# Optimization experiments

Hardware: AMD Instinct MI355X
Metric: run time of the kernel (lower is better)

## Reference

```python
import jax, jax.numpy as jnp
import numpy as np

N, F_IN, F_OUT, K = 16384, 64, 64, 3


def setup_inputs() -> dict:
    key = jax.random.key(0)
    k1, k2, k3, k4 = jax.random.split(key, 4)
    x = jax.random.normal(k1, (N, F_IN), dtype=jnp.float32)
    # dense rescaled Laplacian; scale so repeated matmuls stay numerically tame
    L_tilde = jax.random.normal(k2, (N, N), dtype=jnp.float32) / np.float32(np.sqrt(N))
    stdv = 1.0 / np.sqrt(F_OUT)
    weights = jax.random.uniform(k3, (K + 1, F_IN, F_OUT), dtype=jnp.float32,
                                 minval=-stdv, maxval=stdv)
    bias = jax.random.uniform(k4, (F_OUT,), dtype=jnp.float32, minval=-stdv, maxval=stdv)
    return {"x": x, "L_tilde": L_tilde, "weights": weights, "bias": bias}


def reference(x, L_tilde, weights, bias):
    # Chebyshev recurrence: T0 = x, T1 = L@x, Tk = 2*L@T_{k-1} - T_{k-2}
    T_prev = x                                   # (N, F_in)
    out = T_prev @ weights[0]                    # (N, F_out)
    T_curr = L_tilde @ x
    out = out + T_curr @ weights[1]
    for k in range(2, K + 1):                    # fixed small K: python loop is fine
        T_next = 2.0 * (L_tilde @ T_curr) - T_prev
        out = out + T_next @ weights[k]
        T_prev, T_curr = T_curr, T_next
    return out + bias
```

## Files before the change

kernel.cpp:

```cpp
#include <hip/hip_runtime.h>
#include <cstddef>
#include <cstdint>

#define NN 16384
#define FF 64
#define BM 64
#define BK 64
#define SK 4
#define KQ (NN / SK)
#define NC (KQ / BK)

typedef __attribute__((ext_vector_type(8))) short bf16x8;
typedef __attribute__((ext_vector_type(4))) float f32x4;
typedef unsigned short ushort_t;

#define GLOBAL_AS __attribute__((address_space(1)))
#define LDS_AS    __attribute__((address_space(3)))

#define VMCNT8   asm volatile("s_waitcnt vmcnt(8)" ::: "memory")
#define VMCNT0   asm volatile("s_waitcnt vmcnt(0)" ::: "memory")
#define LGKMCNT0 asm volatile("s_waitcnt lgkmcnt(0)" ::: "memory")
#define SCHEDB   __builtin_amdgcn_sched_barrier(0)
#define BARRIER  __builtin_amdgcn_s_barrier()

__device__ __forceinline__ void f32_split(float f, ushort_t& h, ushort_t& l) {
    unsigned u = __builtin_bit_cast(unsigned, f);
    h = (ushort_t)(u >> 16);
    float hf = __builtin_bit_cast(float, u & 0xFFFF0000u);
    float lo = f - hf;
    l = (ushort_t)(__builtin_bit_cast(unsigned, lo) >> 16);
}

__global__ __launch_bounds__(256) void convT_init(
    const float* __restrict__ X, ushort_t* __restrict__ Th,
    ushort_t* __restrict__ Tl, const float* __restrict__ W0,
    const float* __restrict__ bias, float* __restrict__ out)
{
    __shared__ float S[64][68];
    __shared__ float W[64][64];
    const int t = threadIdx.x;
    const int rb = blockIdx.x * 64;
    {
        const int row = t >> 2;
        const int c0 = (t & 3) * 16;
        const float* src = X + (size_t)(rb + row) * FF + c0;
        *(float4*)&S[row][c0 + 0]  = *(const float4*)(src + 0);
        *(float4*)&S[row][c0 + 4]  = *(const float4*)(src + 4);
        *(float4*)&S[row][c0 + 8]  = *(const float4*)(src + 8);
        *(float4*)&S[row][c0 + 12] = *(const float4*)(src + 12);
        float4* wd = (float4*)&W[0][0];
        const float4* ws = (const float4*)W0;
#pragma unroll
        for (int j = 0; j < 4; ++j) wd[t * 4 + j] = ws[t * 4 + j];
    }
    __syncthreads();
    {
        const int cc = t >> 2;
        const int r0 = (t & 3) * 16;
        ushort_t hh[16], ll[16];
#pragma unroll
        for (int i = 0; i < 16; ++i) f32_split(S[r0 + i][cc], hh[i], ll[i]);
        unsigned wh[8], wl[8];
#pragma unroll
        for (int j = 0; j < 8; ++j) {
            wh[j] = (unsigned)hh[2 * j] | ((unsigned)hh[2 * j + 1] << 16);
            wl[j] = (unsigned)ll[2 * j] | ((unsigned)ll[2 * j + 1] << 16);
        }
        const size_t o = (size_t)cc * NN + rb + r0;
        *(uint4*)(Th + o)     = make_uint4(wh[0], wh[1], wh[2], wh[3]);
        *(uint4*)(Th + o + 8) = make_uint4(wh[4], wh[5], wh[6], wh[7]);
        *(uint4*)(Tl + o)     = make_uint4(wl[0], wl[1], wl[2], wl[3]);
        *(uint4*)(Tl + o + 8) = make_uint4(wl[4], wl[5], wl[6], wl[7]);
    }
    {
        const int row0 = (t >> 3) * 2;
        const int col0 = (t & 7) * 8;
        float acc[2][8];
        const float4 b0 = *(const float4*)(bias + col0);
        const float4 b1 = *(const float4*)(bias + col0 + 4);
#pragma unroll
        for (int r = 0; r < 2; ++r) {
            acc[r][0] = b0.x; acc[r][1] = b0.y; acc[r][2] = b0.z; acc[r][3] = b0.w;
            acc[r][4] = b1.x; acc[r][5] = b1.y; acc[r][6] = b1.z; acc[r][7] = b1.w;
        }
#pragma unroll
        for (int f = 0; f < FF; ++f) {
            const float x0 = S[row0][f];
            const float x1 = S[row0 + 1][f];
            const float4 w0 = *(const float4*)&W[f][col0];
            const float4 w1 = *(const float4*)&W[f][col0 + 4];
            acc[0][0] += x0 * w0.x; acc[0][1] += x0 * w0.y;
            acc[0][2] += x0 * w0.z; acc[0][3] += x0 * w0.w;
            acc[0][4] += x0 * w1.x; acc[0][5] += x0 * w1.y;
            acc[0][6] += x0 * w1.z; acc[0][7] += x0 * w1.w;
            acc[1][0] += x1 * w0.x; acc[1][1] += x1 * w0.y;
            acc[1][2] += x1 * w0.z; acc[1][3] += x1 * w0.w;
            acc[1][4] += x1 * w1.x; acc[1][5] += x1 * w1.y;
            acc[1][6] += x1 * w1.z; acc[1][7] += x1 * w1.w;
        }
#pragma unroll
        for (int r = 0; r < 2; ++r) {
            const size_t o = (size_t)(rb + row0 + r) * FF + col0;
            float4 v0, v1;
            v0.x = acc[r][0]; v0.y = acc[r][1]; v0.z = acc[r][2]; v0.w = acc[r][3];
            v1.x = acc[r][4]; v1.y = acc[r][5]; v1.z = acc[r][6]; v1.w = acc[r][7];
            *(float4*)(out + o) = v0;
            *(float4*)(out + o + 4) = v1;
        }
    }
}

__global__ __launch_bounds__(256) void cheb_gemm_mfma(
    const float* __restrict__ L, const ushort_t* __restrict__ Th,
    const ushort_t* __restrict__ Tl, float* __restrict__ P)
{
    __shared__ ushort_t Ah[2][BM * BK];
    __shared__ ushort_t Al[2][BM * BK];
    __shared__ ushort_t Bh[3][FF * BK];
    __shared__ ushort_t Bl[3][FF * BK];

    const int tid  = threadIdx.x;
    const int lane = tid & 63;
    const int w    = tid >> 6;
    const int s    = blockIdx.x >> 8;
    const int m    = blockIdx.x & 255;
    const int row0g = m * BM;
    const int kbase = s * KQ;

    const int wm = w >> 1, wn = w & 1;
    const int frow = lane & 15;
    const int fk8  = (lane >> 4) * 8;

    const int arow = w * 4 + (lane >> 4);
    const int akq  = lane & 15;
    const int axor = (arow & 7) << 4;

    const ushort_t* Tsrc = (w & 1) ? Tl : Th;
    const int boct0 = (w >> 1) * 4;

    f32x4 acc[2][2];
#pragma unroll
    for (int i = 0; i < 2; ++i)
#pragma unroll
        for (int j = 0; j < 2; ++j) acc[i][j] = (f32x4)0.f;

    float4 vaA[4], vaB[4];

    const float* Labase = L + (size_t)(row0g + arow) * NN + kbase + akq * 4;

#define ISSUE_B(c, sb)                                                          \
    {                                                                           \
        const size_t kc = (size_t)(c) * BK;                                     \
        char* bbase = (char*)((w & 1) ? Bl[sb] : Bh[sb]);                       \
        _Pragma("unroll")                                                       \
        for (int o = 0; o < 4; ++o) {                                           \
            const int oct = boct0 + o;                                          \
            const int col = oct * 8 + (lane >> 3);                              \
            const ushort_t* g = Tsrc + (size_t)col * NN + kbase + kc            \
                                + (((lane & 7) ^ (col & 7)) * 8);               \
            __builtin_amdgcn_global_load_lds((const GLOBAL_AS void*)g,          \
                (LDS_AS void*)(bbase + oct * 1024), 16, 0, 0);                  \
        }                                                                       \
    }

#define LOAD_A(va, c)                                                           \
    {                                                                           \
        const float* g = Labase + (size_t)(c) * BK;                             \
        va[0] = *(const float4*)(g);                                            \
        va[1] = *(const float4*)(g + (size_t)16 * NN);                          \
        va[2] = *(const float4*)(g + (size_t)32 * NN);                          \
        va[3] = *(const float4*)(g + (size_t)48 * NN);                          \
    }

#define CONV_WRITE_A(va, sa)                                                    \
    {                                                                           \
        char* ahb = (char*)Ah[sa];                                              \
        char* alb = (char*)Al[sa];                                              \
        _Pragma("unroll")                                                       \
        for (int p = 0; p < 4; ++p) {                                           \
            const int r = arow + p * 16;                                        \
            ushort_t h0, h1, h2, h3, l0, l1, l2, l3;                            \
            f32_split(va[p].x, h0, l0);                                         \
            f32_split(va[p].y, h1, l1);                                         \
            f32_split(va[p].z, h2, l2);                                         \
            f32_split(va[p].w, h3, l3);                                         \
            const unsigned hi01 = (unsigned)h0 | ((unsigned)h1 << 16);          \
            const unsigned hi23 = (unsigned)h2 | ((unsigned)h3 << 16);          \
            const unsigned lo01 = (unsigned)l0 | ((unsigned)l1 << 16);          \
            const unsigned lo23 = (unsigned)l2 | ((unsigned)l3 << 16);          \
            const int byte = (r * 128 + akq * 8) ^ axor;                        \
            *(uint2*)(ahb + byte) = make_uint2(hi01, hi23);                     \
            *(uint2*)(alb + byte) = make_uint2(lo01, lo23);                     \
        }                                                                       \
    }

#define COMPUTE(sa, sb)                                                         \
    {                                                                           \
        const char* ahb = (const char*)Ah[sa];                                  \
        const char* alb = (const char*)Al[sa];                                  \
        const char* bhb = (const char*)Bh[sb];                                  \
        const char* blb = (const char*)Bl[sb];                                  \
        _Pragma("unroll")                                                       \
        for (int ks = 0; ks < 2; ++ks) {                                        \
            const int kk = ks * 32 + fk8;                                       \
            bf16x8 Afh[2], Afl[2], Bfh[2], Bfl[2];                              \
            _Pragma("unroll")                                                   \
            for (int mt = 0; mt < 2; ++mt) {                                    \
                const int row = wm * 32 + mt * 16 + frow;                       \
                const int off = (row * 128 + kk * 2) ^ ((row & 7) << 4);        \
                Afh[mt] = *(const bf16x8*)(ahb + off);                          \
                Afl[mt] = *(const bf16x8*)(alb + off);                          \
            }                                                                   \
            _Pragma("unroll")                                                   \
            for (int nt = 0; nt < 2; ++nt) {                                    \
                const int col = wn * 32 + nt * 16 + frow;                       \
                const int off = (col * 128 + kk * 2) ^ ((col & 7) << 4);        \
                Bfh[nt] = *(const bf16x8*)(bhb + off);                          \
                Bfl[nt] = *(const bf16x8*)(blb + off);                          \
            }                                                                   \
            _Pragma("unroll")                                                   \
            for (int mt = 0; mt < 2; ++mt)                                      \
                _Pragma("unroll")                                               \
                for (int nt = 0; nt < 2; ++nt) {                                \
                    acc[mt][nt] = __builtin_amdgcn_mfma_f32_16x16x32_bf16(      \
                        Afh[mt], Bfh[nt], acc[mt][nt], 0, 0, 0);                \
                    acc[mt][nt] = __builtin_amdgcn_mfma_f32_16x16x32_bf16(      \
                        Afh[mt], Bfl[nt], acc[mt][nt], 0, 0, 0);                \
                    acc[mt][nt] = __builtin_amdgcn_mfma_f32_16x16x32_bf16(      \
                        Afl[mt], Bfh[nt], acc[mt][nt], 0, 0, 0);                \
                }                                                               \
        }                                                                       \
    }

    LOAD_A(vaA, 0)
    ISSUE_B(0, 0)
    LOAD_A(vaB, 1)
    ISSUE_B(1, 1)
    SCHEDB;
    VMCNT8;
    SCHEDB;
    CONV_WRITE_A(vaA, 0)
    LGKMCNT0;
    BARRIER;
    SCHEDB;

#pragma unroll 1
    for (int c = 0; c < NC; c += 2) {
        if (c + 2 < NC) {
            LOAD_A(vaA, c + 2)
            ISSUE_B(c + 2, (c + 2) % 3)
            SCHEDB;
        }
        COMPUTE(0, c % 3)
        if (c + 2 < NC) { VMCNT8; } else { VMCNT0; }
        SCHEDB;
        CONV_WRITE_A(vaB, 1)
        LGKMCNT0;
        BARRIER;
        SCHEDB;

        if (c + 3 < NC) {
            LOAD_A(vaB, c + 3)
            ISSUE_B(c + 3, (c + 3) % 3)
            SCHEDB;
        }
        COMPUTE(1, (c + 1) % 3)
        if (c + 2 < NC) {
            if (c + 3 < NC) { VMCNT8; } else { VMCNT0; }
            SCHEDB;
            CONV_WRITE_A(vaA, 0)
            LGKMCNT0;
            BARRIER;
            SCHEDB;
        }
    }

    float* Pp = P + (size_t)s * NN * FF;
#pragma unroll
    for (int mt = 0; mt < 2; ++mt)
#pragma unroll
        for (int nt = 0; nt < 2; ++nt) {
            const int row = row0g + wm * 32 + mt * 16 + (lane >> 4) * 4;
            const int col = wn * 32 + nt * 16 + frow;
#pragma unroll
            for (int r = 0; r < 4; ++r)
                Pp[(size_t)(row + r) * FF + col] = acc[mt][nt][r];
        }
#undef ISSUE_B
#undef LOAD_A
#undef CONV_WRITE_A
#undef COMPUTE
}

__global__ __launch_bounds__(256) void post_hop(
    const float* __restrict__ P,
    const float* __restrict__ Tsub, const float* __restrict__ Wk,
    float* __restrict__ Tstore, ushort_t* __restrict__ Thn,
    ushort_t* __restrict__ Tln, float* __restrict__ out,
    float alpha, float beta)
{
    __shared__ float ST[64][33];
    __shared__ float WK[64][64];
    const int t = threadIdx.x;
    const int rb = blockIdx.x * 32;
    const size_t M1 = (size_t)NN * FF;

    {
        float4* wd = (float4*)&WK[0][0];
        const float4* ws = (const float4*)Wk;
#pragma unroll
        for (int j = 0; j < 4; ++j) wd[t * 4 + j] = ws[t * 4 + j];
    }

    const int row = t >> 3;
    const int c0 = (t & 7) * 8;
    const size_t o = (size_t)(rb + row) * FF + c0;

    {
        float tv[8];
#pragma unroll
        for (int half = 0; half < 2; ++half) {
            const size_t oo = o + 4 * half;
            float4 a0 = *(const float4*)(P + oo);
            const float4 a1 = *(const float4*)(P + M1 + oo);
            const float4 a2 = *(const float4*)(P + 2 * M1 + oo);
            const float4 a3 = *(const float4*)(P + 3 * M1 + oo);
            a0.x += a1.x + a2.x + a3.x; a0.y += a1.y + a2.y + a3.y;
            a0.z += a1.z + a2.z + a3.z; a0.w += a1.w + a2.w + a3.w;
            tv[4 * half + 0] = alpha * a0.x; tv[4 * half + 1] = alpha * a0.y;
            tv[4 * half + 2] = alpha * a0.z; tv[4 * half + 3] = alpha * a0.w;
        }
        if (beta != 0.f) {
            const float4 s0 = *(const float4*)(Tsub + o);
            const float4 s1 = *(const float4*)(Tsub + o + 4);
            tv[0] += beta * s0.x; tv[1] += beta * s0.y;
            tv[2] += beta * s0.z; tv[3] += beta * s0.w;
            tv[4] += beta * s1.x; tv[5] += beta * s1.y;
            tv[6] += beta * s1.z; tv[7] += beta * s1.w;
        }
        if (Tstore) {
            float4 v0, v1;
            v0.x = tv[0]; v0.y = tv[1]; v0.z = tv[2]; v0.w = tv[3];
            v1.x = tv[4]; v1.y = tv[5]; v1.z = tv[6]; v1.w = tv[7];
            *(float4*)(Tstore + o) = v0;
            *(float4*)(Tstore + o + 4) = v1;
        }
#pragma unroll
        for (int j = 0; j < 8; ++j) ST[c0 + j][row] = tv[j];
    }
    __syncthreads();

    if (Thn) {
        const int f = t >> 2;
        const int r0 = (t & 3) * 8;
        ushort_t hh[8], ll[8];
#pragma unroll
        for (int i = 0; i < 8; ++i) f32_split(ST[f][r0 + i], hh[i], ll[i]);
        unsigned wh[4], wl[4];
#pragma unroll
        for (int j = 0; j < 4; ++j) {
            wh[j] = (unsigned)hh[2 * j] | ((unsigned)hh[2 * j + 1] << 16);
            wl[j] = (unsigned)ll[2 * j] | ((unsigned)ll[2 * j + 1] << 16);
        }
        const size_t ob = (size_t)f * NN + rb + r0;
        *(uint4*)(Thn + ob) = make_uint4(wh[0], wh[1], wh[2], wh[3]);
        *(uint4*)(Tln + ob) = make_uint4(wl[0], wl[1], wl[2], wl[3]);
    }

    {
        float4 a0 = *(const float4*)(out + o);
        float4 a1 = *(const float4*)(out + o + 4);
#pragma unroll
        for (int f = 0; f < FF; ++f) {
            const float sv = ST[f][row];
            const float4 w0 = *(const float4*)&WK[f][c0];
            const float4 w1 = *(const float4*)&WK[f][c0 + 4];
            a0.x += sv * w0.x; a0.y += sv * w0.y;
            a0.z += sv * w0.z; a0.w += sv * w0.w;
            a1.x += sv * w1.x; a1.y += sv * w1.y;
            a1.z += sv * w1.z; a1.w += sv * w1.w;
        }
        *(float4*)(out + o) = a0;
        *(float4*)(out + o + 4) = a1;
    }
}

extern "C" void kernel_launch(void* const* d_in, const int* in_sizes, int n_in,
                              void* d_out, int out_size, void* d_ws, size_t ws_size,
                              hipStream_t stream)
{
    const float* x    = (const float*)d_in[0];
    const float* L    = (const float*)d_in[1];
    const float* W    = (const float*)d_in[2];
    const float* bias = (const float*)d_in[3];
    float* out = (float*)d_out;

    const size_t M1 = (size_t)NN * FF;
    float* wsf = (float*)d_ws;
    float* T1 = wsf;
    float* P  = wsf + M1;
    ushort_t* ThA = (ushort_t*)(wsf + 5 * M1);
    ushort_t* TlA = ThA + M1;
    ushort_t* ThB = TlA + M1;
    ushort_t* TlB = ThB + M1;

    const dim3 gc(NN / 64), bc(256);
    const dim3 gg(SK * 256), bg(256);
    const dim3 gp(NN / 32), bp(256);

    convT_init<<<gc, bc, 0, stream>>>(x, ThA, TlA, W + 0 * FF * FF, bias, out);
    cheb_gemm_mfma<<<gg, bg, 0, stream>>>(L, ThA, TlA, P);
    post_hop<<<gp, bp, 0, stream>>>(P, x, W + 1 * FF * FF,
                                    T1, ThB, TlB, out, 1.f, 0.f);
    cheb_gemm_mfma<<<gg, bg, 0, stream>>>(L, ThB, TlB, P);
    post_hop<<<gp, bp, 0, stream>>>(P, x, W + 2 * FF * FF,
                                    nullptr, ThA, TlA, out, 2.f, -1.f);
    cheb_gemm_mfma<<<gg, bg, 0, stream>>>(L, ThA, TlA, P);
    post_hop<<<gp, bp, 0, stream>>>(P, T1, W + 3 * FF * FF,
                                    nullptr, nullptr, nullptr, out, 2.f, -1.f);
}
```

Baseline: 763.8 us.

## Restructure GEMM pipeline to load A chunk pairs and double-buffer B

The split-K GEMM main loop is rewritten so each A register load fetches two consecutive K-chunks (8 float4 per thread), and B shrinks from triple to double buffering in LDS. Hand-placed vmcnt/lgkmcnt waits and sched barriers give way to plain __syncthreads. The goal is fewer, wider global loads in flight and lower LDS use, which may allow more resident blocks. The cost is higher register pressure and the loss of fine-grained wait control, which could expose memory latency.

New measurement: 693.8 us (median of 2 runs). -9.2%, faster.

```diff
diff --git a/kernel.cpp b/kernel.cpp
--- a/kernel.cpp
+++ b/kernel.cpp
@@ -16,12 +16,6 @@
 
 #define GLOBAL_AS __attribute__((address_space(1)))
 #define LDS_AS    __attribute__((address_space(3)))
-
-#define VMCNT8   asm volatile("s_waitcnt vmcnt(8)" ::: "memory")
-#define VMCNT0   asm volatile("s_waitcnt vmcnt(0)" ::: "memory")
-#define LGKMCNT0 asm volatile("s_waitcnt lgkmcnt(0)" ::: "memory")
-#define SCHEDB   __builtin_amdgcn_sched_barrier(0)
-#define BARRIER  __builtin_amdgcn_s_barrier()
 
 __device__ __forceinline__ void f32_split(float f, ushort_t& h, ushort_t& l) {
     unsigned u = __builtin_bit_cast(unsigned, f);
@@ -116,8 +110,8 @@
 {
     __shared__ ushort_t Ah[2][BM * BK];
     __shared__ ushort_t Al[2][BM * BK];
-    __shared__ ushort_t Bh[3][FF * BK];
-    __shared__ ushort_t Bl[3][FF * BK];
+    __shared__ ushort_t Bh[2][FF * BK];
+    __shared__ ushort_t Bl[2][FF * BK];
 
     const int tid  = threadIdx.x;
     const int lane = tid & 63;
@@ -144,14 +138,14 @@
 #pragma unroll
         for (int j = 0; j < 2; ++j) acc[i][j] = (f32x4)0.f;
 
-    float4 vaA[4], vaB[4];
+    float4 vaA[8], vaB[8];
 
     const float* Labase = L + (size_t)(row0g + arow) * NN + kbase + akq * 4;
 
-#define ISSUE_B(c, sb)                                                          \
+#define ISSUE_B(c, slot)                                                        \
     {                                                                           \
         const size_t kc = (size_t)(c) * BK;                                     \
-        char* bbase = (char*)((w & 1) ? Bl[sb] : Bh[sb]);                       \
+        char* bbase = (char*)((w & 1) ? Bl[slot] : Bh[slot]);                   \
         _Pragma("unroll")                                                       \
         for (int o = 0; o < 4; ++o) {                                           \
             const int oct = boct0 + o;                                          \
@@ -163,27 +157,32 @@
         }                                                                       \
     }
 
-#define LOAD_A(va, c)                                                           \
+#define LOAD_PAIR(va, c)                                                        \
     {                                                                           \
         const float* g = Labase + (size_t)(c) * BK;                             \
         va[0] = *(const float4*)(g);                                            \
-        va[1] = *(const float4*)(g + (size_t)16 * NN);                          \
-        va[2] = *(const float4*)(g + (size_t)32 * NN);                          \
-        va[3] = *(const float4*)(g + (size_t)48 * NN);                          \
-    }
-
-#define CONV_WRITE_A(va, sa)                                                    \
+        va[1] = *(const float4*)(g + BK);                                       \
+        va[2] = *(const float4*)(g + (size_t)16 * NN);                          \
+        va[3] = *(const float4*)(g + (size_t)16 * NN + BK);                     \
+        va[4] = *(const float4*)(g + (size_t)32 * NN);                          \
+        va[5] = *(const float4*)(g + (size_t)32 * NN + BK);                     \
+        va[6] = *(const float4*)(g + (size_t)48 * NN);                          \
+        va[7] = *(const float4*)(g + (size_t)48 * NN + BK);                     \
+    }
+
+#define CONV_WRITE_A(va, j, slot)                                               \
     {                                                                           \
-        char* ahb = (char*)Ah[sa];                                              \
-        char* alb = (char*)Al[sa];                                              \
+        char* ahb = (char*)Ah[slot];                                            \
+        char* alb = (char*)Al[slot];                                            \
         _Pragma("unroll")                                                       \
         for (int p = 0; p < 4; ++p) {                                           \
+            const float4 v = va[p * 2 + (j)];                                   \
             const int r = arow + p * 16;                                        \
             ushort_t h0, h1, h2, h3, l0, l1, l2, l3;                            \
-            f32_split(va[p].x, h0, l0);                                         \
-            f32_split(va[p].y, h1, l1);                                         \
-            f32_split(va[p].z, h2, l2);                                         \
-            f32_split(va[p].w, h3, l3);                                         \
+            f32_split(v.x, h0, l0);                                             \
+            f32_split(v.y, h1, l1);                                             \
+            f32_split(v.z, h2, l2);                                             \
+            f32_split(v.w, h3, l3);                                             \
             const unsigned hi01 = (unsigned)h0 | ((unsigned)h1 << 16);          \
             const unsigned hi23 = (unsigned)h2 | ((unsigned)h3 << 16);          \
             const unsigned lo01 = (unsigned)l0 | ((unsigned)l1 << 16);          \
@@ -194,12 +193,12 @@
         }                                                                       \
     }
 
-#define COMPUTE(sa, sb)                                                         \
+#define COMPUTE(slot)                                                           \
     {                                                                           \
-        const char* ahb = (const char*)Ah[sa];                                  \
-        const char* alb = (const char*)Al[sa];                                  \
-        const char* bhb = (const char*)Bh[sb];                                  \
-        const char* blb = (const char*)Bl[sb];                                  \
+        const char* ahb = (const char*)Ah[slot];                                \
+        const char* alb = (const char*)Al[slot];                                \
+        const char* bhb = (const char*)Bh[slot];                                \
+        const char* blb = (const char*)Bl[slot];                                \
         _Pragma("unroll")                                                       \
         for (int ks = 0; ks < 2; ++ks) {                                        \
             const int kk = ks * 32 + fk8;                                       \
@@ -232,47 +231,32 @@
         }                                                                       \
     }
 
-    LOAD_A(vaA, 0)
     ISSUE_B(0, 0)
-    LOAD_A(vaB, 1)
-    ISSUE_B(1, 1)
-    SCHEDB;
-    VMCNT8;
-    SCHEDB;
-    CONV_WRITE_A(vaA, 0)
-    LGKMCNT0;
-    BARRIER;
-    SCHEDB;
+    LOAD_PAIR(vaA, 0)
+    CONV_WRITE_A(vaA, 0, 0)
+    __syncthreads();
 
 #pragma unroll 1
-    for (int c = 0; c < NC; c += 2) {
-        if (c + 2 < NC) {
-            LOAD_A(vaA, c + 2)
-            ISSUE_B(c + 2, (c + 2) % 3)
-            SCHEDB;
-        }
-        COMPUTE(0, c % 3)
-        if (c + 2 < NC) { VMCNT8; } else { VMCNT0; }
-        SCHEDB;
-        CONV_WRITE_A(vaB, 1)
-        LGKMCNT0;
-        BARRIER;
-        SCHEDB;
-
-        if (c + 3 < NC) {
-            LOAD_A(vaB, c + 3)
-            ISSUE_B(c + 3, (c + 3) % 3)
-            SCHEDB;
-        }
-        COMPUTE(1, (c + 1) % 3)
-        if (c + 2 < NC) {
-            if (c + 3 < NC) { VMCNT8; } else { VMCNT0; }
-            SCHEDB;
-            CONV_WRITE_A(vaA, 0)
-            LGKMCNT0;
-            BARRIER;
-            SCHEDB;
-        }
+    for (int c = 0; c < NC; c += 4) {
+        ISSUE_B(c + 1, 1)
+        if (c + 2 < NC) LOAD_PAIR(vaB, c + 2)
+        COMPUTE(0)
+        CONV_WRITE_A(vaA, 1, 1)
+        __syncthreads();
+        if (c + 2 < NC) ISSUE_B(c + 2, 0)
+        COMPUTE(1)
+        if (c + 2 < NC) CONV_WRITE_A(vaB, 0, 0)
+        __syncthreads();
+        if (c + 2 >= NC) break;
+        ISSUE_B(c + 3, 1)
+        if (c + 4 < NC) LOAD_PAIR(vaA, c + 4)
+        COMPUTE(0)
+        CONV_WRITE_A(vaB, 1, 1)
+        __syncthreads();
+        if (c + 4 < NC) ISSUE_B(c + 4, 0)
+        COMPUTE(1)
+        if (c + 4 < NC) CONV_WRITE_A(vaA, 0, 0)
+        __syncthreads();
     }
 
     float* Pp = P + (size_t)s * NN * FF;
@@ -287,7 +271,7 @@
                 Pp[(size_t)(row + r) * FF + col] = acc[mt][nt][r];
         }
 #undef ISSUE_B
-#undef LOAD_A
+#undef LOAD_PAIR
 #undef CONV_WRITE_A
 #undef COMPUTE
 }
```
